# Kernel optimization log

Hardware: AMD Instinct MI355X
Metric: run time of the kernel (lower is better)

The kernel has to match this reference:

```python
import jax, jax.numpy as jnp
import numpy as np

N_NODES = 100000
N_EDGES = 3200000


def _spmm(rows, cols, vals, x):
    # out[i] = sum_{e: rows[e]==i} vals[e] * x[cols[e]]
    msgs = vals[:, None] * x[cols]  # [E, F]
    return jax.ops.segment_sum(msgs, rows, num_segments=N_NODES)


def setup_inputs() -> dict:
    key = jax.random.key(0)
    ks = jax.random.split(key, 8)
    x = jax.random.normal(ks[0], (N_NODES, 256), dtype=jnp.float32)
    adj_rows = jax.random.randint(ks[1], (N_EDGES,), 0, N_NODES, dtype=jnp.int32)
    adj_cols = jax.random.randint(ks[2], (N_EDGES,), 0, N_NODES, dtype=jnp.int32)
    adj_vals = jax.random.uniform(ks[3], (N_EDGES,), dtype=jnp.float32)
    W1 = jax.random.normal(ks[4], (256, 128), dtype=jnp.float32) * (1.0 / np.sqrt(256))
    b1 = jnp.zeros((128,), dtype=jnp.float32)
    W2 = jax.random.normal(ks[5], (128, 64), dtype=jnp.float32) * (1.0 / np.sqrt(128))
    b2 = jnp.zeros((64,), dtype=jnp.float32)
    return {"x": x, "adj_rows": adj_rows, "adj_cols": adj_cols, "adj_vals": adj_vals,
            "W1": W1, "b1": b1, "W2": W2, "b2": b2}


def reference(x, adj_rows, adj_cols, adj_vals, W1, b1, W2, b2):
    # Layer 0: spmm -> linear -> relu (dropout inactive in eval)
    h = _spmm(adj_rows, adj_cols, adj_vals, x)
    h = jax.nn.relu(h @ W1 + b1)
    # Layer 1 (last layer): spmm -> linear, no activation
    h = _spmm(adj_rows, adj_cols, adj_vals, h)
    out = h @ W2 + b2
    return out  # squeeze(1) is a no-op for [N, nclass]
```

## Files before the change

kernel.cpp:

```cpp
#include <hip/hip_runtime.h>
#include <hip/hip_fp16.h>


#define RPB 480
#define NB_MAX 1024
#define PCHUNK 8192
#define EPT 32
#define CAP_SHIFT 14
#define CAP (1 << CAP_SHIFT)

typedef _Float16 half8 __attribute__((ext_vector_type(8)));
typedef _Float16 h2t __attribute__((ext_vector_type(2)));
typedef float floatx4 __attribute__((ext_vector_type(4)));

__global__ __launch_bounds__(256) void prep_weights_kernel(const float* __restrict__ W1,
                                                           const float* __restrict__ W2,
                                                           __half* __restrict__ W1T,
                                                           h2t* __restrict__ pk,
                                                           int* __restrict__ gcnt) {
    int i = blockIdx.x * 256 + threadIdx.x;
    if (i < 256 * 128) {
        int k = i >> 7, n = i & 127;
        W1T[n * 256 + k] = __float2half_rn(W1[i]);
    } else if (i < 256 * 128 + 4096) {
        int j = i - 256 * 128;
        int kk = j >> 6, c = j & 63;
        h2t v;
        v[0] = (_Float16)W2[(2 * kk) * 64 + c];
        v[1] = (_Float16)W2[(2 * kk + 1) * 64 + c];
        pk[j] = v;
    } else {
        int j = i - (256 * 128 + 4096);
        if (j < NB_MAX) gcnt[j] = 0;
    }
}

__global__ __launch_bounds__(256) void transpose_w_kernel(const float* __restrict__ W,
                                                          __half* __restrict__ WT,
                                                          int K, int N) {
    int i = blockIdx.x * 256 + threadIdx.x;
    if (i < K * N) {
        int k = i / N, n = i % N;
        WT[n * K + k] = __float2half_rn(W[i]);
    }
}

__global__ __launch_bounds__(256) void partition_kernel(const int* __restrict__ rows,
                                                        const int* __restrict__ cols,
                                                        const float* __restrict__ vals,
                                                        int* __restrict__ gcnt,
                                                        int2* __restrict__ eb1,
                                                        int nE, int nB) {
    __shared__ int hist[NB_MAX];
    __shared__ int cur[NB_MAX];
    const int t = threadIdx.x;
    const int c0 = blockIdx.x * PCHUNK;
    for (int b = t; b < nB; b += 256) hist[b] = 0;
    __syncthreads();
    int myr[EPT];
#pragma unroll
    for (int j = 0; j < EPT; ++j) {
        int e = c0 + t + 256 * j;
        int r = (e < nE) ? rows[e] : -1;
        myr[j] = r;
        if (r >= 0) atomicAdd(&hist[r / RPB], 1);
    }
    __syncthreads();
    for (int b = t; b < nB; b += 256) {
        int c = hist[b];
        cur[b] = c ? (b << CAP_SHIFT) + atomicAdd(&gcnt[b], c) : 0;
    }
    __syncthreads();
#pragma unroll
    for (int j = 0; j < EPT; ++j) {
        int r = myr[j];
        if (r >= 0) {
            int e = c0 + t + 256 * j;
            int bk = r / RPB;
            int rl = r - bk * RPB;
            int pos = atomicAdd(&cur[bk], 1);
            if (pos < ((bk + 1) << CAP_SHIFT))
                eb1[pos] = make_int2((cols[e] & 0x1FFFF) | (rl << 17), __float_as_int(vals[e]));
        }
    }
}

__global__ __launch_bounds__(1024) void fine_scatter_kernel(const int* __restrict__ gcnt,
                                                            const int2* __restrict__ eb1,
                                                            int2* __restrict__ eb2,
                                                            int2* __restrict__ off2,
                                                            int nN) {
    __shared__ int hist[RPB];
    __shared__ int sc[RPB];
    __shared__ int cur[RPB];
    const int b = blockIdx.x;
    const int row0 = b * RPB;
    const int nr = min(RPB, nN - row0);
    const int t = threadIdx.x;
    const int s = b << CAP_SHIFT;
    const int e = s + min(gcnt[b], CAP);

    if (t < RPB) hist[t] = 0;
    __syncthreads();
    for (int i = s + t; i < e; i += 1024)
        atomicAdd(&hist[((unsigned)eb1[i].x) >> 17], 1);
    __syncthreads();

    int myc = (t < RPB) ? hist[t] : 0;
    if (t < RPB) sc[t] = myc;
    __syncthreads();
    for (int d = 1; d < RPB; d <<= 1) {
        int add = (t < RPB && t >= d) ? sc[t - d] : 0;
        __syncthreads();
        if (t < RPB) sc[t] += add;
        __syncthreads();
    }
    if (t < RPB) {
        int excl = s + sc[t] - myc;
        cur[t] = excl;
        if (t < nr) off2[row0 + t] = make_int2(excl, myc);
    }
    __syncthreads();

    for (int i = s + t; i < e; i += 1024) {
        int2 ed = eb1[i];
        unsigned x = (unsigned)ed.x;
        int pos = atomicAdd(&cur[x >> 17], 1);
        eb2[pos] = make_int2((int)(x & 0x1FFFF), ed.y);
    }
}

__global__ __launch_bounds__(256) void spmm_fused_kernel(const int2* __restrict__ off2,
                                                         const int2* __restrict__ eb,
                                                         const __half* __restrict__ Y,
                                                         const float* __restrict__ b1,
                                                         const h2t* __restrict__ pk,
                                                         __half* __restrict__ Y2, int nN) {
    __shared__ h2t w2s[64 * 64];
    __shared__ h2t hs[4][64];
    const int t = threadIdx.x;
#pragma unroll
    for (int i = 0; i < 16; ++i) w2s[i * 256 + t] = pk[i * 256 + t];
    __syncthreads();

    const int wv = t >> 6;
    const int lane = t & 63;
    const int fg = lane & 15;
    const int g = lane >> 4;
    const int gw = blockIdx.x * 4 + wv;
    const int nw = gridDim.x * 4;

    for (int row = gw; row < nN; row += nw) {
        float acc[8];
#pragma unroll
        for (int p = 0; p < 8; ++p) acc[p] = 0.f;

        int2 se = off2[row];
        int s = se.x;
        int e1 = s + se.y;
        for (int base = s; base < e1; base += 64) {
            int n = min(64, e1 - base);
            int2 my = (lane < n) ? eb[base + lane] : make_int2(0, 0);
            for (int j = 0; j < n; j += 8) {
                int i0 = j + g;
                int i1 = j + 4 + g;
                int s0 = (i0 < n) ? i0 : j;
                int s1 = (i1 < n) ? i1 : j;
                int c0 = __shfl(my.x, s0);
                int c1 = __shfl(my.x, s1);
                float v0 = __int_as_float(__shfl(my.y, s0));
                float v1 = __int_as_float(__shfl(my.y, s1));
                if (i0 >= n) v0 = 0.f;
                if (i1 >= n) v1 = 0.f;
                half8 y0 = *(const half8*)(Y + ((size_t)c0 << 7) + (fg << 3));
                half8 y1 = *(const half8*)(Y + ((size_t)c1 << 7) + (fg << 3));
#pragma unroll
                for (int p = 0; p < 8; ++p) acc[p] = fmaf(v0, (float)y0[p], acc[p]);
#pragma unroll
                for (int p = 0; p < 8; ++p) acc[p] = fmaf(v1, (float)y1[p], acc[p]);
            }
        }
#pragma unroll
        for (int p = 0; p < 8; ++p) acc[p] += __shfl_xor(acc[p], 16);
#pragma unroll
        for (int p = 0; p < 8; ++p) acc[p] += __shfl_xor(acc[p], 32);

        if (g == 0) {
            floatx4 ba = *(const floatx4*)(b1 + fg * 8);
            floatx4 bb = *(const floatx4*)(b1 + fg * 8 + 4);
            float f[8];
#pragma unroll
            for (int p = 0; p < 4; ++p) f[p] = fmaxf(acc[p] + ba[p], 0.f);
#pragma unroll
            for (int p = 0; p < 4; ++p) f[4 + p] = fmaxf(acc[4 + p] + bb[p], 0.f);
#pragma unroll
            for (int p = 0; p < 4; ++p) {
                h2t pr;
                pr[0] = (_Float16)f[2 * p];
                pr[1] = (_Float16)f[2 * p + 1];
                hs[wv][fg * 4 + p] = pr;
            }
        }
        __builtin_amdgcn_sched_barrier(0);

        float o = 0.f;
#pragma unroll 8
        for (int kk = 0; kk < 64; ++kk) {
            h2t a = hs[wv][kk];
            h2t b = w2s[kk * 64 + lane];
#if __has_builtin(__builtin_amdgcn_fdot2)
            o = __builtin_amdgcn_fdot2(a, b, o, false);
#else
            o = fmaf((float)a[0], (float)b[0], o);
            o = fmaf((float)a[1], (float)b[1], o);
#endif
        }
        Y2[(size_t)row * 64 + lane] = __float2half_rn(o);
    }
}

__global__ __launch_bounds__(256) void spmm_csr64_kernel(const int2* __restrict__ off2,
                                                         const int2* __restrict__ eb,
                                                         const __half* __restrict__ Y,
                                                         const float* __restrict__ bias,
                                                         float* __restrict__ out, int nN) {
    const int lane = threadIdx.x & 63;
    const int fg = lane & 7;
    const int g = lane >> 3;
    const int gw = blockIdx.x * 4 + (threadIdx.x >> 6);
    const int nw = gridDim.x * 4;

    for (int row = gw; row < nN; row += nw) {
        float acc[8];
#pragma unroll
        for (int p = 0; p < 8; ++p) acc[p] = 0.f;

        int2 se = off2[row];
        int s = se.x;
        int e1 = s + se.y;
        for (int base = s; base < e1; base += 64) {
            int n = min(64, e1 - base);
            int2 my = (lane < n) ? eb[base + lane] : make_int2(0, 0);
            for (int j = 0; j < n; j += 16) {
                int i0 = j + g;
                int i1 = j + 8 + g;
                int s0 = (i0 < n) ? i0 : j;
                int s1 = (i1 < n) ? i1 : j;
                int c0 = __shfl(my.x, s0);
                int c1 = __shfl(my.x, s1);
                float v0 = __int_as_float(__shfl(my.y, s0));
                float v1 = __int_as_float(__shfl(my.y, s1));
                if (i0 >= n) v0 = 0.f;
                if (i1 >= n) v1 = 0.f;
                half8 y0 = *(const half8*)(Y + ((size_t)c0 << 6) + (fg << 3));
                half8 y1 = *(const half8*)(Y + ((size_t)c1 << 6) + (fg << 3));
#pragma unroll
                for (int p = 0; p < 8; ++p) acc[p] = fmaf(v0, (float)y0[p], acc[p]);
#pragma unroll
                for (int p = 0; p < 8; ++p) acc[p] = fmaf(v1, (float)y1[p], acc[p]);
            }
        }
#pragma unroll
        for (int p = 0; p < 8; ++p) acc[p] += __shfl_xor(acc[p], 8);
#pragma unroll
        for (int p = 0; p < 8; ++p) acc[p] += __shfl_xor(acc[p], 16);
#pragma unroll
        for (int p = 0; p < 8; ++p) acc[p] += __shfl_xor(acc[p], 32);

        if (g == 0) {
            floatx4 ba = *(const floatx4*)(bias + fg * 8);
            floatx4 bb = *(const floatx4*)(bias + fg * 8 + 4);
            floatx4 o0, o1;
#pragma unroll
            for (int p = 0; p < 4; ++p) o0[p] = acc[p] + ba[p];
#pragma unroll
            for (int p = 0; p < 4; ++p) o1[p] = acc[4 + p] + bb[p];
            float* op = out + (size_t)row * 64 + fg * 8;
            *(floatx4*)op = o0;
            *(floatx4*)(op + 4) = o1;
        }
    }
}

__global__ __launch_bounds__(256) void init_bias_kernel(float* __restrict__ out,
                                                        const float* __restrict__ bias,
                                                        int fmask, size_t total) {
    size_t i = (size_t)blockIdx.x * 256 + threadIdx.x;
    if (i < total) out[i] = bias[i & fmask];
}

template <int F>
__global__ __launch_bounds__(256) void spmm_atomic_kernel(const int* __restrict__ rows,
                                                          const int* __restrict__ cols,
                                                          const float* __restrict__ vals,
                                                          const __half* __restrict__ Y,
                                                          float* __restrict__ out, int nE) {
    int e = blockIdx.x * 4 + (threadIdx.x >> 6);
    if (e >= nE) return;
    int lane = threadIdx.x & 63;
    int r = rows[e];
    int c = cols[e];
    float v = vals[e];
    if (F == 128) {
        float2 y = __half22float2(*((const __half2*)(Y + (size_t)c * 128) + lane));
        float* op = out + (size_t)r * 128 + lane * 2;
        unsafeAtomicAdd(op, v * y.x);
        unsafeAtomicAdd(op + 1, v * y.y);
    } else {
        float y = __half2float(Y[(size_t)c * F + lane]);
        unsafeAtomicAdd(out + (size_t)r * F + lane, v * y);
    }
}

template <int NN, int KK, bool RELU_IN>
__global__ __launch_bounds__(256) void gemm_mfma_kernel(const float* __restrict__ A,
                                                        const __half* __restrict__ BT,
                                                        __half* __restrict__ C, int nrows) {
    constexpr int MT = 64, KT = 64, KP = KT + 8;
    __shared__ __half As[MT * KP];
    __shared__ __half Bs[NN * KP];
    const int tid = threadIdx.x;
    const int wid = tid >> 6, lane = tid & 63;
    const int row0 = blockIdx.x * MT;
    const int wr = wid & 1, wc = wid >> 1;
    constexpr int WCT = NN / 32;
    const int lrow = lane & 15, q = lane >> 4;

    floatx4 acc[2][WCT];
#pragma unroll
    for (int rt = 0; rt < 2; ++rt)
#pragma unroll
        for (int ct = 0; ct < WCT; ++ct)
#pragma unroll
            for (int i = 0; i < 4; ++i) acc[rt][ct][i] = 0.f;

    for (int kt = 0; kt < KK; kt += KT) {
#pragma unroll
        for (int it = 0; it < MT * KT / 4 / 256; ++it) {
            int i4 = it * 256 + tid;
            int m = i4 >> 4;
            int kk = (i4 & 15) << 2;
            int gr = row0 + m;
            float4 v = make_float4(0.f, 0.f, 0.f, 0.f);
            if (gr < nrows) v = *(const float4*)(A + (size_t)gr * KK + kt + kk);
            if (RELU_IN) {
                v.x = fmaxf(v.x, 0.f); v.y = fmaxf(v.y, 0.f);
                v.z = fmaxf(v.z, 0.f); v.w = fmaxf(v.w, 0.f);
            }
            __half h0 = __float2half_rn(v.x), h1 = __float2half_rn(v.y);
            __half h2 = __float2half_rn(v.z), h3 = __float2half_rn(v.w);
            ushort4 u = make_ushort4(*(unsigned short*)&h0, *(unsigned short*)&h1,
                                     *(unsigned short*)&h2, *(unsigned short*)&h3);
            *(ushort4*)(As + m * KP + kk) = u;
        }
#pragma unroll
        for (int it = 0; it < NN * KT / 4 / 256; ++it) {
            int i4 = it * 256 + tid;
            int n = i4 >> 4;
            int kk = (i4 & 15) << 2;
            *(ushort4*)(Bs + n * KP + kk) =
                *(const ushort4*)(BT + (size_t)n * KK + kt + kk);
        }
        __syncthreads();

#pragma unroll
        for (int ks = 0; ks < KT; ks += 32) {
            half8 a0 = *(half8*)(As + (wr * 32 + lrow) * KP + ks + q * 8);
            half8 a1 = *(half8*)(As + (wr * 32 + 16 + lrow) * KP + ks + q * 8);
#pragma unroll
            for (int ct = 0; ct < WCT; ++ct) {
                half8 b = *(half8*)(Bs + (wc * (NN / 2) + ct * 16 + lrow) * KP + ks + q * 8);
                acc[0][ct] = __builtin_amdgcn_mfma_f32_16x16x32_f16(a0, b, acc[0][ct], 0, 0, 0);
                acc[1][ct] = __builtin_amdgcn_mfma_f32_16x16x32_f16(a1, b, acc[1][ct], 0, 0, 0);
            }
        }
        __syncthreads();
    }

#pragma unroll
    for (int rt = 0; rt < 2; ++rt)
#pragma unroll
        for (int ct = 0; ct < WCT; ++ct)
#pragma unroll
            for (int r = 0; r < 4; ++r) {
                int gr = row0 + wr * 32 + rt * 16 + q * 4 + r;
                if (gr < nrows)
                    C[(size_t)gr * NN + wc * (NN / 2) + ct * 16 + lrow] =
                        __float2half_rn(acc[rt][ct][r]);
            }
}

extern "C" void kernel_launch(void* const* d_in, const int* in_sizes, int n_in,
                              void* d_out, int out_size, void* d_ws, size_t ws_size,
                              hipStream_t stream) {
    const float* x    = (const float*)d_in[0];
    const int*   rows = (const int*)d_in[1];
    const int*   cols = (const int*)d_in[2];
    const float* vals = (const float*)d_in[3];
    const float* W1   = (const float*)d_in[4];
    const float* b1   = (const float*)d_in[5];
    const float* W2   = (const float*)d_in[6];
    const float* b2   = (const float*)d_in[7];
    float* out = (float*)d_out;

    const int nN = in_sizes[0] / 256;
    const int nE = in_sizes[1];
    const int nB = (nN + RPB - 1) / RPB;

    const int mblocks  = (nN + 63) / 64;
    const int pblocks  = (nE + PCHUNK - 1) / PCHUNK;
    const int sblocks  = min(2048, (nN + 3) / 4);
    const int eblocks4 = (nE + 3) / 4;

    char* w = (char*)d_ws;
    __half* Y1h  = (__half*)w;  w += (size_t)nN * 128 * 2;
    __half* Y2h  = (__half*)w;  w += (size_t)nN * 64 * 2;
    __half* W1T  = (__half*)w;  w += (size_t)256 * 128 * 2;
    h2t*    pk   = (h2t*)w;     w += (size_t)4096 * 4;
    int2*   off2 = (int2*)w;    w += (size_t)nN * 8;
    int*    gcnt = (int*)w;     w += (size_t)NB_MAX * 4;
    int2*   eb1  = (int2*)w;    w += ((size_t)nB << CAP_SHIFT) * 8;
    int2*   eb2  = (int2*)w;    w += ((size_t)nB << CAP_SHIFT) * 8;
    size_t need = (size_t)(w - (char*)d_ws);

    const bool slots_ok = (nE / nB) <= (CAP - 1050);

    if (ws_size >= need && nN <= (1 << 17) && nB <= NB_MAX && slots_ok) {
        prep_weights_kernel<<<(256 * 128 + 4096 + NB_MAX + 255) / 256, 256, 0, stream>>>(
            W1, W2, W1T, pk, gcnt);
        gemm_mfma_kernel<128, 256, false><<<mblocks, 256, 0, stream>>>(x, W1T, Y1h, nN);

        partition_kernel<<<pblocks, 256, 0, stream>>>(rows, cols, vals, gcnt, eb1, nE, nB);
        fine_scatter_kernel<<<nB, 1024, 0, stream>>>(gcnt, eb1, eb2, off2, nN);

        spmm_fused_kernel<<<sblocks, 256, 0, stream>>>(off2, eb2, Y1h, b1, pk, Y2h, nN);
        spmm_csr64_kernel<<<sblocks, 256, 0, stream>>>(off2, eb2, Y2h, b2, out, nN);
    } else {
        char* v = (char*)d_ws;
        __half* fY1h = (__half*)v;  v += (size_t)nN * 128 * 2;
        float*  fH1  = (float*)v;   v += (size_t)nN * 128 * 4;
        __half* fW1T = (__half*)v;  v += (size_t)256 * 128 * 2;
        __half* fW2T = (__half*)v;  v += (size_t)128 * 64 * 2;

        transpose_w_kernel<<<(256 * 128 + 255) / 256, 256, 0, stream>>>(W1, fW1T, 256, 128);
        transpose_w_kernel<<<(128 * 64 + 255) / 256, 256, 0, stream>>>(W2, fW2T, 128, 64);
        gemm_mfma_kernel<128, 256, false><<<mblocks, 256, 0, stream>>>(x, fW1T, fY1h, nN);
        size_t totH1 = (size_t)nN * 128;
        init_bias_kernel<<<(int)((totH1 + 255) / 256), 256, 0, stream>>>(fH1, b1, 127, totH1);
        spmm_atomic_kernel<128><<<eblocks4, 256, 0, stream>>>(rows, cols, vals, fY1h, fH1, nE);
        gemm_mfma_kernel<64, 128, true><<<mblocks, 256, 0, stream>>>(fH1, fW2T, fY1h, nN);
        size_t totOut = (size_t)nN * 64;
        init_bias_kernel<<<(int)((totOut + 255) / 256), 256, 0, stream>>>(out, b2, 63, totOut);
        spmm_atomic_kernel<64><<<eblocks4, 256, 0, stream>>>(rows, cols, vals, fY1h, out, nE);
    }
}
```

Measured before the change: 463.1 us.

## Merge first GEMM and edge partition into one heterogeneous kernel launch

Combines the dense x@W1 MFMA GEMM and the edge bucket-partition pass into a single launch, where the first pblocks blocks partition edges and the remaining blocks compute GEMM tiles. The two independent stages can then run concurrently on the GPU, mixing a compute-bound job with a memory/atomic-bound one and removing one launch boundary. In exchange, both paths share one dynamic shared-memory size and register budget, which may lower occupancy for the partition blocks, and the GEMM tiling is reimplemented inline (64-row tiles).

New measurement: 450.4 us. 1.03x faster.

```diff
diff --git a/kernel.cpp b/kernel.cpp
--- a/kernel.cpp
+++ b/kernel.cpp
@@ -45,43 +45,116 @@
     }
 }
 
-__global__ __launch_bounds__(256) void partition_kernel(const int* __restrict__ rows,
-                                                        const int* __restrict__ cols,
-                                                        const float* __restrict__ vals,
-                                                        int* __restrict__ gcnt,
-                                                        int2* __restrict__ eb1,
-                                                        int nE, int nB) {
-    __shared__ int hist[NB_MAX];
-    __shared__ int cur[NB_MAX];
+__global__ __launch_bounds__(256) void gemm_part_kernel(
+    const float* __restrict__ A, const __half* __restrict__ BT,
+    __half* __restrict__ C, int nrows,
+    const int* __restrict__ rows, const int* __restrict__ cols,
+    const float* __restrict__ vals, int* __restrict__ gcnt,
+    int2* __restrict__ eb1, int nE, int nB, int pblocks) {
+    extern __shared__ char smem[];
     const int t = threadIdx.x;
-    const int c0 = blockIdx.x * PCHUNK;
-    for (int b = t; b < nB; b += 256) hist[b] = 0;
-    __syncthreads();
-    int myr[EPT];
-#pragma unroll
-    for (int j = 0; j < EPT; ++j) {
-        int e = c0 + t + 256 * j;
-        int r = (e < nE) ? rows[e] : -1;
-        myr[j] = r;
-        if (r >= 0) atomicAdd(&hist[r / RPB], 1);
-    }
-    __syncthreads();
-    for (int b = t; b < nB; b += 256) {
-        int c = hist[b];
-        cur[b] = c ? (b << CAP_SHIFT) + atomicAdd(&gcnt[b], c) : 0;
-    }
-    __syncthreads();
-#pragma unroll
-    for (int j = 0; j < EPT; ++j) {
-        int r = myr[j];
-        if (r >= 0) {
+
+    if ((int)blockIdx.x < pblocks) {
+        int* hist = (int*)smem;
+        int* cur = hist + NB_MAX;
+        const int c0 = blockIdx.x * PCHUNK;
+        for (int b = t; b < nB; b += 256) hist[b] = 0;
+        __syncthreads();
+        int myr[EPT];
+#pragma unroll
+        for (int j = 0; j < EPT; ++j) {
             int e = c0 + t + 256 * j;
-            int bk = r / RPB;
-            int rl = r - bk * RPB;
-            int pos = atomicAdd(&cur[bk], 1);
-            if (pos < ((bk + 1) << CAP_SHIFT))
-                eb1[pos] = make_int2((cols[e] & 0x1FFFF) | (rl << 17), __float_as_int(vals[e]));
-        }
+            int r = (e < nE) ? rows[e] : -1;
+            myr[j] = r;
+            if (r >= 0) atomicAdd(&hist[r / RPB], 1);
+        }
+        __syncthreads();
+        for (int b = t; b < nB; b += 256) {
+            int c = hist[b];
+            cur[b] = c ? (b << CAP_SHIFT) + atomicAdd(&gcnt[b], c) : 0;
+        }
+        __syncthreads();
+#pragma unroll
+        for (int j = 0; j < EPT; ++j) {
+            int r = myr[j];
+            if (r >= 0) {
+                int e = c0 + t + 256 * j;
+                int bk = r / RPB;
+                int rl = r - bk * RPB;
+                int pos = atomicAdd(&cur[bk], 1);
+                if (pos < ((bk + 1) << CAP_SHIFT))
+                    eb1[pos] = make_int2((cols[e] & 0x1FFFF) | (rl << 17),
+                                         __float_as_int(vals[e]));
+            }
+        }
+    } else {
+        constexpr int MT = 64, KT = 64, KP = KT + 8, NN = 128, KK = 256;
+        constexpr int WCT = NN / 32;
+        __half* As = (__half*)smem;
+        __half* Bs = As + MT * KP;
+        const int wid = t >> 6, lane = t & 63;
+        const int row0 = ((int)blockIdx.x - pblocks) * MT;
+        const int wr = wid & 1, wc = wid >> 1;
+        const int lrow = lane & 15, q = lane >> 4;
+
+        floatx4 acc[2][WCT];
+#pragma unroll
+        for (int rt = 0; rt < 2; ++rt)
+#pragma unroll
+            for (int ct = 0; ct < WCT; ++ct)
+#pragma unroll
+                for (int i = 0; i < 4; ++i) acc[rt][ct][i] = 0.f;
+
+        for (int kt = 0; kt < KK; kt += KT) {
+#pragma unroll
+            for (int it = 0; it < MT * KT / 4 / 256; ++it) {
+                int i4 = it * 256 + t;
+                int m = i4 >> 4;
+                int kk = (i4 & 15) << 2;
+                int gr = row0 + m;
+                float4 v = make_float4(0.f, 0.f, 0.f, 0.f);
+                if (gr < nrows) v = *(const float4*)(A + (size_t)gr * KK + kt + kk);
+                __half h0 = __float2half_rn(v.x), h1 = __float2half_rn(v.y);
+                __half h2 = __float2half_rn(v.z), h3 = __float2half_rn(v.w);
+                ushort4 u = make_ushort4(*(unsigned short*)&h0, *(unsigned short*)&h1,
+                                         *(unsigned short*)&h2, *(unsigned short*)&h3);
+                *(ushort4*)(As + m * KP + kk) = u;
+            }
+#pragma unroll
+            for (int it = 0; it < NN * KT / 4 / 256; ++it) {
+                int i4 = it * 256 + t;
+                int n = i4 >> 4;
+                int kk = (i4 & 15) << 2;
+                *(ushort4*)(Bs + n * KP + kk) =
+                    *(const ushort4*)(BT + (size_t)n * KK + kt + kk);
+            }
+            __syncthreads();
+
+#pragma unroll
+            for (int ks = 0; ks < KT; ks += 32) {
+                half8 a0 = *(half8*)(As + (wr * 32 + lrow) * KP + ks + q * 8);
+                half8 a1 = *(half8*)(As + (wr * 32 + 16 + lrow) * KP + ks + q * 8);
+#pragma unroll
+                for (int ct = 0; ct < WCT; ++ct) {
+                    half8 b = *(half8*)(Bs + (wc * (NN / 2) + ct * 16 + lrow) * KP + ks + q * 8);
+                    acc[0][ct] = __builtin_amdgcn_mfma_f32_16x16x32_f16(a0, b, acc[0][ct], 0, 0, 0);
+                    acc[1][ct] = __builtin_amdgcn_mfma_f32_16x16x32_f16(a1, b, acc[1][ct], 0, 0, 0);
+                }
+            }
+            __syncthreads();
+        }
+
+#pragma unroll
+        for (int rt = 0; rt < 2; ++rt)
+#pragma unroll
+            for (int ct = 0; ct < WCT; ++ct)
+#pragma unroll
+                for (int r = 0; r < 4; ++r) {
+                    int gr = row0 + wr * 32 + rt * 16 + q * 4 + r;
+                    if (gr < nrows)
+                        C[(size_t)gr * NN + wc * (NN / 2) + ct * 16 + lrow] =
+                            __float2half_rn(acc[rt][ct][r]);
+                }
     }
 }
 
@@ -428,9 +501,10 @@
     if (ws_size >= need && nN <= (1 << 17) && nB <= NB_MAX && slots_ok) {
         prep_weights_kernel<<<(256 * 128 + 4096 + NB_MAX + 255) / 256, 256, 0, stream>>>(
             W1, W2, W1T, pk, gcnt);
-        gemm_mfma_kernel<128, 256, false><<<mblocks, 256, 0, stream>>>(x, W1T, Y1h, nN);
-
-        partition_kernel<<<pblocks, 256, 0, stream>>>(rows, cols, vals, gcnt, eb1, nE, nB);
+
+        gemm_part_kernel<<<pblocks + mblocks, 256, (64 + 128) * 72 * 2, stream>>>(
+            x, W1T, Y1h, nN, rows, cols, vals, gcnt, eb1, nE, nB, pblocks);
+
         fine_scatter_kernel<<<nB, 1024, 0, stream>>>(gcnt, eb1, eb2, off2, nN);
 
         spmm_fused_kernel<<<sblocks, 256, 0, stream>>>(off2, eb2, Y1h, b1, pk, Y2h, nN);
```
